# Performance work log

Measured on AMD Instinct MI355X. Metric: run time of the kernel, lower is better.

Reference implementation:

```python
import math
import jax, jax.numpy as jnp
import numpy as np

SHAPES = ((100, 150), (50, 75), (25, 38), (13, 19))  # (H, W) per level
N_HEADS = 8
N_POINTS = 4
EMBED = 256


def setup_inputs() -> dict:
    key = jax.random.key(0)
    ks = jax.random.split(key, 8)
    bs = 2
    L = len(SHAPES)
    nv = sum(h * w for h, w in SHAPES)  # 19947
    nq = nv
    d = EMBED
    query = jax.random.normal(ks[0], (bs, nq, d), jnp.float32)
    value = jax.random.normal(ks[1], (bs, nv, d), jnp.float32)
    reference_points = jax.random.uniform(ks[2], (bs, nq, L, 2), dtype=jnp.float32)
    spatial_shapes = jnp.asarray(np.array(SHAPES, np.int32))
    # sampling_offsets bias: directional grid init, as in the module's init_weights
    thetas = np.arange(N_HEADS, dtype=np.float64) * (2.0 * math.pi / N_HEADS)
    grid = np.stack([np.cos(thetas), np.sin(thetas)], -1)
    grid = grid / np.abs(grid).max(-1, keepdims=True)
    grid = np.tile(grid[:, None, None, :], (1, L, N_POINTS, 1))
    grid = grid * np.arange(1, N_POINTS + 1, dtype=np.float64)[None, None, :, None]
    b_off = jnp.asarray(grid.reshape(-1), jnp.float32)  # (h*L*p*2,)
    # small random weights (zero-init in module would make offsets constant)
    W_off = 0.01 * jax.random.normal(ks[3], (N_HEADS * L * N_POINTS * 2, d), jnp.float32)
    W_attn = 0.01 * jax.random.normal(ks[4], (N_HEADS * L * N_POINTS, d), jnp.float32)
    b_attn = jnp.zeros((N_HEADS * L * N_POINTS,), jnp.float32)
    s = 1.0 / math.sqrt(d)
    W_val = s * jax.random.normal(ks[5], (d, d), jnp.float32)
    b_val = jnp.zeros((d,), jnp.float32)
    W_out = s * jax.random.normal(ks[6], (d, d), jnp.float32)
    b_out = jnp.zeros((d,), jnp.float32)
    return dict(query=query, value=value, reference_points=reference_points,
                spatial_shapes=spatial_shapes, W_off=W_off, b_off=b_off,
                W_attn=W_attn, b_attn=b_attn, W_val=W_val, b_val=b_val,
                W_out=W_out, b_out=b_out)


def _msda(value, shapes, loc, attn):
    """Multi-scale deformable attention core.
    value: (bs, nv, h, hd)  loc: (bs, nq, h, L, p, 2) in [0,1]
    attn:  (bs, nq, h, L, p) -> returns (bs, nq, h*hd)
    Equivalent to grid_sample(bilinear, padding='zeros', align_corners=False).
    """
    bs, nq, h, L, p, _ = loc.shape
    hd = value.shape[-1]
    out = jnp.zeros((bs, nq, h, hd), value.dtype)
    start = 0
    for lvl in range(L):
        H, W = int(shapes[lvl, 0]), int(shapes[lvl, 1])
        v = value[:, start:start + H * W]               # (bs, H*W, h, hd)
        l = loc[:, :, :, lvl]                           # (bs, nq, h, p, 2)
        # align_corners=False unnormalization: x = loc*W - 0.5
        x = l[..., 0] * W - 0.5
        y = l[..., 1] * H - 0.5
        x0 = jnp.floor(x)
        y0 = jnp.floor(y)
        wx = x - x0
        wy = y - y0
        x0i = x0.astype(jnp.int32)
        y0i = y0.astype(jnp.int32)

        def corner(xi, yi, w):
            valid = (xi >= 0) & (xi < W) & (yi >= 0) & (yi < H)
            idx = jnp.clip(yi, 0, H - 1) * W + jnp.clip(xi, 0, W - 1)  # (bs,nq,h,p)
            idxf = idx.transpose(0, 1, 3, 2).reshape(bs, nq * p, h)
            g = jnp.take_along_axis(v, idxf[..., None], axis=1)        # (bs,nq*p,h,hd)
            g = g.reshape(bs, nq, p, h, hd).transpose(0, 1, 3, 2, 4)   # (bs,nq,h,p,hd)
            return g * jnp.where(valid, w, 0.0)[..., None]

        samp = (corner(x0i, y0i, (1 - wx) * (1 - wy))
                + corner(x0i + 1, y0i, wx * (1 - wy))
                + corner(x0i, y0i + 1, (1 - wx) * wy)
                + corner(x0i + 1, y0i + 1, wx * wy))
        out = out + (samp * attn[:, :, :, lvl, :, None]).sum(3)
        start += H * W
    return out.reshape(bs, nq, h * hd)


def reference(query, value, reference_points, spatial_shapes,
              W_off, b_off, W_attn, b_attn, W_val, b_val, W_out, b_out):
    shapes = np.asarray(spatial_shapes)  # static level shapes
    bs, nq, d = query.shape
    L = shapes.shape[0]
    h, p = N_HEADS, N_POINTS
    hd = d // h
    off = (query @ W_off.T + b_off).reshape(bs, nq, h, L, p, 2)
    aw = (query @ W_attn.T + b_attn).reshape(bs, nq, h, L * p)
    aw = jax.nn.softmax(aw, axis=-1).reshape(bs, nq, h, L, p)
    v = (value @ W_val.T + b_val).reshape(bs, -1, h, hd)
    # offset normalizer is (W, H) per level
    norm = jnp.asarray(np.stack([shapes[:, 1], shapes[:, 0]], -1), query.dtype)  # (L,2)
    loc = reference_points[:, :, None, :, None, :] + off / norm[None, None, None, :, None, :]
    out = _msda(v, shapes, loc, aw)          # (bs, nq, d)
    return out @ W_out.T + b_out
```

## Files before the change

kernel.cpp:

```cpp
#include <hip/hip_runtime.h>
#include <hip/hip_bf16.h>
#include <hip/hip_fp16.h>
#include <cmath>


typedef __attribute__((ext_vector_type(8))) short short8;
typedef __attribute__((ext_vector_type(4))) float f32x4;

#define MREAL 39894
#define MP    39936
#define NQ2   39894

__device__ __forceinline__ unsigned short f2bf(float f) {
    union { float f; unsigned u; } x; x.f = f;
    unsigned r = (x.u + 0x7fffu + ((x.u >> 16) & 1u)) >> 16;
    return (unsigned short)r;
}
__device__ __forceinline__ unsigned cvt_pk_bf16(float lo, float hi) {
    unsigned r;
    asm("v_cvt_pk_bf16_f32 %0, %1, %2" : "=v"(r) : "v"(lo), "v"(hi));
    return r;
}

__global__ __launch_bounds__(256) void cast_w4(
    const float* __restrict__ woff, const float* __restrict__ wattn,
    const float* __restrict__ wval, const float* __restrict__ wout,
    short* __restrict__ wb)
{
    int c = blockIdx.x * 256 + threadIdx.x;
    const float* s; short* d; int off;
    if (c < 8192)       { s = woff;  d = wb;          off = c; }
    else if (c < 12288) { s = wattn; d = wb + 65536;  off = c - 8192; }
    else if (c < 20480) { s = wval;  d = wb + 98304;  off = c - 12288; }
    else                { s = wout;  d = wb + 163840; off = c - 20480; }
    const float4* f4 = reinterpret_cast<const float4*>(s) + (size_t)off * 2;
    float4 a = f4[0], b = f4[1];
    short8 o;
    o[0] = (short)f2bf(a.x); o[1] = (short)f2bf(a.y);
    o[2] = (short)f2bf(a.z); o[3] = (short)f2bf(a.w);
    o[4] = (short)f2bf(b.x); o[5] = (short)f2bf(b.y);
    o[6] = (short)f2bf(b.z); o[7] = (short)f2bf(b.w);
    *reinterpret_cast<short8*>(d + (size_t)off * 8) = o;
}

template<int AMODE, int OUTMODE, int NT>
__global__ __launch_bounds__(256) void gemm_bf16_nt(
    const void* __restrict__ A, const short* __restrict__ B,
    const float* __restrict__ bias, const float* __restrict__ bias2, int bsplit,
    void* __restrict__ Cout, int ldc, int c0, int Mstore)
{
    __shared__ short As[128 * 40];
    __shared__ short Bs[128 * 40];

    const int bid = blockIdx.x;
    const int m_t = ((bid / (8 * NT)) << 3) | (bid & 7);
    const int n_t = (bid >> 3) % NT;
    const int m0 = m_t * 128;
    const int n0 = n_t * 128;

    const int tid = threadIdx.x;
    const int w  = tid >> 6;
    const int l  = tid & 63;
    const int wm = w >> 1, wn = w & 1;

    const int sr  = tid >> 2;
    const int skc = (tid & 3) * 8;

    const int lr = l & 15;
    const int lk = (l >> 4) * 8;

    f32x4 acc[4][4] = {};

    for (int k0 = 0; k0 < 256; k0 += 32) {
        __syncthreads();
        if constexpr (AMODE == 0) {
            const short* Ab = (const short*)A;
            *reinterpret_cast<short8*>(&As[sr * 40 + skc]) =
                *reinterpret_cast<const short8*>(&Ab[(size_t)(m0 + sr) * 256 + k0 + skc]);
            *reinterpret_cast<short8*>(&As[(sr + 64) * 40 + skc]) =
                *reinterpret_cast<const short8*>(&Ab[(size_t)(m0 + sr + 64) * 256 + k0 + skc]);
        } else {
            const float* Af = (const float*)A;
            const int r0 = min(m0 + sr, MREAL - 1);
            const int r1 = min(m0 + sr + 64, MREAL - 1);
            float4 a0 = *reinterpret_cast<const float4*>(&Af[(size_t)r0 * 256 + k0 + skc]);
            float4 a1 = *reinterpret_cast<const float4*>(&Af[(size_t)r0 * 256 + k0 + skc + 4]);
            float4 b0 = *reinterpret_cast<const float4*>(&Af[(size_t)r1 * 256 + k0 + skc]);
            float4 b1 = *reinterpret_cast<const float4*>(&Af[(size_t)r1 * 256 + k0 + skc + 4]);
            uint4 pa, pb;
            pa.x = cvt_pk_bf16(a0.x, a0.y); pa.y = cvt_pk_bf16(a0.z, a0.w);
            pa.z = cvt_pk_bf16(a1.x, a1.y); pa.w = cvt_pk_bf16(a1.z, a1.w);
            pb.x = cvt_pk_bf16(b0.x, b0.y); pb.y = cvt_pk_bf16(b0.z, b0.w);
            pb.z = cvt_pk_bf16(b1.x, b1.y); pb.w = cvt_pk_bf16(b1.z, b1.w);
            *reinterpret_cast<uint4*>(&As[sr * 40 + skc]) = pa;
            *reinterpret_cast<uint4*>(&As[(sr + 64) * 40 + skc]) = pb;
        }
        *reinterpret_cast<short8*>(&Bs[sr * 40 + skc]) =
            *reinterpret_cast<const short8*>(&B[(size_t)(n0 + sr) * 256 + k0 + skc]);
        *reinterpret_cast<short8*>(&Bs[(sr + 64) * 40 + skc]) =
            *reinterpret_cast<const short8*>(&B[(size_t)(n0 + sr + 64) * 256 + k0 + skc]);
        __syncthreads();

        short8 bfr[4];
#pragma unroll
        for (int ni = 0; ni < 4; ++ni)
            bfr[ni] = *reinterpret_cast<const short8*>(&Bs[(wn * 64 + ni * 16 + lr) * 40 + lk]);
#pragma unroll
        for (int mi = 0; mi < 4; ++mi) {
            short8 afr = *reinterpret_cast<const short8*>(&As[(wm * 64 + mi * 16 + lr) * 40 + lk]);
#pragma unroll
            for (int ni = 0; ni < 4; ++ni)
                acc[mi][ni] = __builtin_amdgcn_mfma_f32_16x16x32_bf16(afr, bfr[ni], acc[mi][ni], 0, 0, 0);
        }
    }

    const int r4 = (l >> 4) * 4;
#pragma unroll
    for (int ni = 0; ni < 4; ++ni) {
        const int col = n0 + wn * 64 + ni * 16 + lr;
        const float bv = (col < bsplit) ? bias[col] : bias2[col - bsplit];
#pragma unroll
        for (int mi = 0; mi < 4; ++mi) {
#pragma unroll
            for (int r = 0; r < 4; ++r) {
                const int row = m0 + wm * 64 + mi * 16 + r4 + r;
                if (row < Mstore) {
                    const float val = acc[mi][ni][r] + bv;
                    if constexpr (OUTMODE == 2) {
                        union { __half h; unsigned short u; } cv; cv.h = __float2half(val);
                        reinterpret_cast<unsigned short*>(Cout)[(size_t)row * ldc + c0 + col] = cv.u;
                    } else if constexpr (OUTMODE == 3) {
                        union { __half h; unsigned short u; } cv; cv.h = __float2half(val);
                        reinterpret_cast<unsigned short*>(Cout)[(size_t)(col >> 5) * MP * 32
                                                               + (size_t)row * 32 + (col & 31)] = cv.u;
                    } else {
                        reinterpret_cast<float*>(Cout)[(size_t)row * ldc + c0 + col] = val;
                    }
                }
            }
        }
    }
}

__global__ __launch_bounds__(256) void msda_sample6(
    const char* __restrict__ vplanes,
    const __half* __restrict__ offattn,
    const float* __restrict__ ref,
    uint4* __restrict__ sampled)
{
    __shared__ __attribute__((aligned(16))) unsigned s_w[16][68];
    __shared__ __attribute__((aligned(16))) int      s_idx[16][68];
    __shared__ float s_e[16][17];
    __shared__ float s_inv[16];

    const int bid = blockIdx.x;
    const int h = bid & 7;
    const int qbase = (bid >> 3) * 16;
    const int tid = threadIdx.x;
    const int qp = tid >> 4;

    {
        const int s = tid & 15;
        const int lvl = s >> 2;
        const int qi = qbase + qp;
        const bool live = (qi < NQ2);

        const int Hs[4] = {100, 50, 25, 13};
        const int Ws[4] = {150, 75, 38, 19};
        const int st[4] = {0, 15000, 18750, 19700};

        float e = 1.f;
        unsigned wv[4] = {0, 0, 0, 0};
        int      iv[4] = {0, 0, 0, 0};
        if (live) {
            const __half* oa = offattn + (size_t)qi * 384;
            unsigned short lu = __builtin_nontemporal_load(
                reinterpret_cast<const unsigned short*>(oa + 256 + h * 16 + s));
            union { unsigned short u; __half h; } lh; lh.u = lu;
            e = expf(__half2float(lh.h));
            unsigned ou = __builtin_nontemporal_load(
                reinterpret_cast<const unsigned*>(oa + h * 32 + 2 * s));
            union { unsigned u; __half2 h2; } oh; oh.u = ou;
            const float ox = __low2float(oh.h2), oy = __high2float(oh.h2);
            const float2 r2 = *reinterpret_cast<const float2*>(ref + (size_t)qi * 8 + lvl * 2);

            const int H = Hs[lvl], W = Ws[lvl];
            const float x = r2.x * (float)W + ox - 0.5f;
            const float y = r2.y * (float)H + oy - 0.5f;
            const float x0f = floorf(x), y0f = floorf(y);
            const float wx = x - x0f, wy = y - y0f;
            const int x0 = (int)x0f, y0 = (int)y0f;
            const int base = ((qi >= 19947) ? 19947 : 0) + st[lvl];

            const float w00 = (1.f - wx) * (1.f - wy), w01 = wx * (1.f - wy);
            const float w10 = (1.f - wx) * wy,         w11 = wx * wy;
            const bool vx0 = (x0 >= 0) & (x0 < W), vx1 = (x0 + 1 >= 0) & (x0 + 1 < W);
            const bool vy0 = (y0 >= 0) & (y0 < H), vy1 = (y0 + 1 >= 0) & (y0 + 1 < H);
            const int xc0 = min(max(x0, 0), W - 1), xc1 = min(max(x0 + 1, 0), W - 1);
            const int yc0 = min(max(y0, 0), H - 1), yc1 = min(max(y0 + 1, 0), H - 1);
            iv[0] = (base + yc0 * W + xc0) << 6;
            iv[1] = (base + yc0 * W + xc1) << 6;
            iv[2] = (base + yc1 * W + xc0) << 6;
            iv[3] = (base + yc1 * W + xc1) << 6;
            union { __half2 h; unsigned u; } cw;
            cw.h = __float2half2_rn((vx0 & vy0) ? e * w00 : 0.f); wv[0] = cw.u;
            cw.h = __float2half2_rn((vx1 & vy0) ? e * w01 : 0.f); wv[1] = cw.u;
            cw.h = __float2half2_rn((vx0 & vy1) ? e * w10 : 0.f); wv[2] = cw.u;
            cw.h = __float2half2_rn((vx1 & vy1) ? e * w11 : 0.f); wv[3] = cw.u;
        }
        s_e[qp][s] = e;
#pragma unroll
        for (int c = 0; c < 4; ++c) {
            s_w[qp][c * 16 + s] = wv[c];
            s_idx[qp][c * 16 + s] = iv[c];
        }
    }
    __syncthreads();

    if (tid < 16) {
        float d = 0.f;
#pragma unroll
        for (int i = 0; i < 16; ++i) d += s_e[tid][i];
        s_inv[tid] = 1.f / d;
    }
    __syncthreads();

    const int l = tid & 63;
    const int c4 = (l >> 2) & 3;
    const int cp4 = l & 3;
    const int qi = qbase + qp;

    const char* vb = vplanes + (size_t)h * (MP * 64) + cp4 * 16;

    union HU { __half2 h; unsigned u; };
    __half2 acc[4];
#pragma unroll
    for (int i = 0; i < 4; ++i) acc[i] = __float2half2_rn(0.f);

    const unsigned* wp = &s_w[qp][c4 * 16];
    const int*      ip = &s_idx[qp][c4 * 16];

#pragma unroll
    for (int k = 0; k < 4; ++k) {
        const uint4 w4 = *reinterpret_cast<const uint4*>(wp + k * 4);
        const int4  i4 = *reinterpret_cast<const int4*>(ip + k * 4);
        const uint4 p0 = *reinterpret_cast<const uint4*>(vb + i4.x);
        const uint4 p1 = *reinterpret_cast<const uint4*>(vb + i4.y);
        const uint4 p2 = *reinterpret_cast<const uint4*>(vb + i4.z);
        const uint4 p3 = *reinterpret_cast<const uint4*>(vb + i4.w);
        HU va, ww;
        ww.u = w4.x;
        va.u = p0.x; acc[0] = __hfma2(va.h, ww.h, acc[0]);
        va.u = p0.y; acc[1] = __hfma2(va.h, ww.h, acc[1]);
        va.u = p0.z; acc[2] = __hfma2(va.h, ww.h, acc[2]);
        va.u = p0.w; acc[3] = __hfma2(va.h, ww.h, acc[3]);
        ww.u = w4.y;
        va.u = p1.x; acc[0] = __hfma2(va.h, ww.h, acc[0]);
        va.u = p1.y; acc[1] = __hfma2(va.h, ww.h, acc[1]);
        va.u = p1.z; acc[2] = __hfma2(va.h, ww.h, acc[2]);
        va.u = p1.w; acc[3] = __hfma2(va.h, ww.h, acc[3]);
        ww.u = w4.z;
        va.u = p2.x; acc[0] = __hfma2(va.h, ww.h, acc[0]);
        va.u = p2.y; acc[1] = __hfma2(va.h, ww.h, acc[1]);
        va.u = p2.z; acc[2] = __hfma2(va.h, ww.h, acc[2]);
        va.u = p2.w; acc[3] = __hfma2(va.h, ww.h, acc[3]);
        ww.u = w4.w;
        va.u = p3.x; acc[0] = __hfma2(va.h, ww.h, acc[0]);
        va.u = p3.y; acc[1] = __hfma2(va.h, ww.h, acc[1]);
        va.u = p3.z; acc[2] = __hfma2(va.h, ww.h, acc[2]);
        va.u = p3.w; acc[3] = __hfma2(va.h, ww.h, acc[3]);
    }

#pragma unroll
    for (int i = 0; i < 4; ++i) {
        HU a; a.h = acc[i];
        HU b;
        b.u = __shfl_xor(a.u, 4, 64); a.h = __hadd2(a.h, b.h);
        b.u = __shfl_xor(a.u, 8, 64); a.h = __hadd2(a.h, b.h);
        acc[i] = a.h;
    }

    if (c4 == 0 && qi < NQ2) {
        const float inv = s_inv[qp];
        uint4 o;
        o.x = ((unsigned)f2bf(__high2float(acc[0]) * inv) << 16) | (unsigned)f2bf(__low2float(acc[0]) * inv);
        o.y = ((unsigned)f2bf(__high2float(acc[1]) * inv) << 16) | (unsigned)f2bf(__low2float(acc[1]) * inv);
        o.z = ((unsigned)f2bf(__high2float(acc[2]) * inv) << 16) | (unsigned)f2bf(__low2float(acc[2]) * inv);
        o.w = ((unsigned)f2bf(__high2float(acc[3]) * inv) << 16) | (unsigned)f2bf(__low2float(acc[3]) * inv);
        sampled[(size_t)qi * 32 + h * 4 + cp4] = o;
    }
}

extern "C" void kernel_launch(void* const* d_in, const int* in_sizes, int n_in,
                              void* d_out, int out_size, void* d_ws, size_t ws_size,
                              hipStream_t stream) {
    const float* query  = (const float*)d_in[0];
    const float* value  = (const float*)d_in[1];
    const float* refp   = (const float*)d_in[2];
    const float* W_off  = (const float*)d_in[4];
    const float* b_off  = (const float*)d_in[5];
    const float* W_attn = (const float*)d_in[6];
    const float* b_attn = (const float*)d_in[7];
    const float* W_val  = (const float*)d_in[8];
    const float* b_val  = (const float*)d_in[9];
    const float* W_out  = (const float*)d_in[10];
    const float* b_out  = (const float*)d_in[11];
    float* out = (float*)d_out;

    short* wb    = (short*)d_ws;
    short* vbuf  = wb + 262144;
    short* oabuf = vbuf + (size_t)MP * 256;
    short* sbuf  = oabuf + (size_t)MP * 384;

    const dim3 blk(256);

    cast_w4<<<dim3(112), blk, 0, stream>>>(W_off, W_attn, W_val, W_out, wb);

    gemm_bf16_nt<1, 3, 2><<<dim3(312 * 2), blk, 0, stream>>>(
        value, wb + 98304, b_val, b_val, 1 << 30, vbuf, 256, 0, MP);
    gemm_bf16_nt<1, 2, 3><<<dim3(312 * 3), blk, 0, stream>>>(
        query, wb, b_off, b_attn, 256, oabuf, 384, 0, MP);

    const int ngroups = (MREAL + 15) / 16;
    msda_sample6<<<dim3(ngroups * 8), blk, 0, stream>>>(
        (const char*)vbuf, (const __half*)oabuf, refp, (uint4*)sbuf);

    gemm_bf16_nt<0, 0, 2><<<dim3(312 * 2), blk, 0, stream>>>(
        sbuf, wb + 163840, b_out, b_out, 1 << 30, out, 256, 0, MREAL);
}
```

Baseline: 170.7 us.

## Fuse weight casting into GEMMs, merge input GEMMs, streamline sampling kernel

Drops the separate weight-cast kernel: the GEMMs now load fp32 weights and convert them to bf16 while staging into shared memory. The value and query projections run as one launch that dispatches on block index. In the sampling kernel, the softmax denominator is now a wave shuffle reduction instead of a shared-memory pass with an extra barrier, expf becomes __expf, and all 16 gathers are issued before any FMAs to raise memory-level parallelism. The cost is redundant fp32 weight loads and conversions in every GEMM block, plus more live registers in the sampler.

```diff
diff --git a/kernel.cpp b/kernel.cpp
--- a/kernel.cpp
+++ b/kernel.cpp
@@ -22,43 +22,16 @@
     return r;
 }
 
-__global__ __launch_bounds__(256) void cast_w4(
-    const float* __restrict__ woff, const float* __restrict__ wattn,
-    const float* __restrict__ wval, const float* __restrict__ wout,
-    short* __restrict__ wb)
+template<int AMODE, int OUTMODE>
+__device__ __forceinline__ void gemm_body(
+    short* As, short* Bs,
+    const void* A, const float* B1, const float* B2, int nsplit,
+    const float* bias, const float* bias2, int bsplit,
+    void* Cout, int ldc, int m_t, int n_t, int Mstore)
 {
-    int c = blockIdx.x * 256 + threadIdx.x;
-    const float* s; short* d; int off;
-    if (c < 8192)       { s = woff;  d = wb;          off = c; }
-    else if (c < 12288) { s = wattn; d = wb + 65536;  off = c - 8192; }
-    else if (c < 20480) { s = wval;  d = wb + 98304;  off = c - 12288; }
-    else                { s = wout;  d = wb + 163840; off = c - 20480; }
-    const float4* f4 = reinterpret_cast<const float4*>(s) + (size_t)off * 2;
-    float4 a = f4[0], b = f4[1];
-    short8 o;
-    o[0] = (short)f2bf(a.x); o[1] = (short)f2bf(a.y);
-    o[2] = (short)f2bf(a.z); o[3] = (short)f2bf(a.w);
-    o[4] = (short)f2bf(b.x); o[5] = (short)f2bf(b.y);
-    o[6] = (short)f2bf(b.z); o[7] = (short)f2bf(b.w);
-    *reinterpret_cast<short8*>(d + (size_t)off * 8) = o;
-}
-
-template<int AMODE, int OUTMODE, int NT>
-__global__ __launch_bounds__(256) void gemm_bf16_nt(
-    const void* __restrict__ A, const short* __restrict__ B,
-    const float* __restrict__ bias, const float* __restrict__ bias2, int bsplit,
-    void* __restrict__ Cout, int ldc, int c0, int Mstore)
-{
-    __shared__ short As[128 * 40];
-    __shared__ short Bs[128 * 40];
-
-    const int bid = blockIdx.x;
-    const int m_t = ((bid / (8 * NT)) << 3) | (bid & 7);
-    const int n_t = (bid >> 3) % NT;
+    const int tid = threadIdx.x;
     const int m0 = m_t * 128;
     const int n0 = n_t * 128;
-
-    const int tid = threadIdx.x;
     const int w  = tid >> 6;
     const int l  = tid & 63;
     const int wm = w >> 1, wn = w & 1;
@@ -68,6 +41,12 @@
 
     const int lr = l & 15;
     const int lk = (l >> 4) * 8;
+
+    const int br0 = n0 + sr, br1 = n0 + sr + 64;
+    const float* Bp0 = (br0 < nsplit) ? B1 + (size_t)br0 * 256
+                                      : B2 + (size_t)(br0 - nsplit) * 256;
+    const float* Bp1 = (br1 < nsplit) ? B1 + (size_t)br1 * 256
+                                      : B2 + (size_t)(br1 - nsplit) * 256;
 
     f32x4 acc[4][4] = {};
 
@@ -95,10 +74,19 @@
             *reinterpret_cast<uint4*>(&As[sr * 40 + skc]) = pa;
             *reinterpret_cast<uint4*>(&As[(sr + 64) * 40 + skc]) = pb;
         }
-        *reinterpret_cast<short8*>(&Bs[sr * 40 + skc]) =
-            *reinterpret_cast<const short8*>(&B[(size_t)(n0 + sr) * 256 + k0 + skc]);
-        *reinterpret_cast<short8*>(&Bs[(sr + 64) * 40 + skc]) =
-            *reinterpret_cast<const short8*>(&B[(size_t)(n0 + sr + 64) * 256 + k0 + skc]);
+        {
+            float4 c0 = *reinterpret_cast<const float4*>(Bp0 + k0 + skc);
+            float4 c1 = *reinterpret_cast<const float4*>(Bp0 + k0 + skc + 4);
+            float4 d0 = *reinterpret_cast<const float4*>(Bp1 + k0 + skc);
+            float4 d1 = *reinterpret_cast<const float4*>(Bp1 + k0 + skc + 4);
+            uint4 pc, pd;
+            pc.x = cvt_pk_bf16(c0.x, c0.y); pc.y = cvt_pk_bf16(c0.z, c0.w);
+            pc.z = cvt_pk_bf16(c1.x, c1.y); pc.w = cvt_pk_bf16(c1.z, c1.w);
+            pd.x = cvt_pk_bf16(d0.x, d0.y); pd.y = cvt_pk_bf16(d0.z, d0.w);
+            pd.z = cvt_pk_bf16(d1.x, d1.y); pd.w = cvt_pk_bf16(d1.z, d1.w);
+            *reinterpret_cast<uint4*>(&Bs[sr * 40 + skc]) = pc;
+            *reinterpret_cast<uint4*>(&Bs[(sr + 64) * 40 + skc]) = pd;
+        }
         __syncthreads();
 
         short8 bfr[4];
@@ -128,13 +116,13 @@
                     const float val = acc[mi][ni][r] + bv;
                     if constexpr (OUTMODE == 2) {
                         union { __half h; unsigned short u; } cv; cv.h = __float2half(val);
-                        reinterpret_cast<unsigned short*>(Cout)[(size_t)row * ldc + c0 + col] = cv.u;
+                        reinterpret_cast<unsigned short*>(Cout)[(size_t)row * ldc + col] = cv.u;
                     } else if constexpr (OUTMODE == 3) {
                         union { __half h; unsigned short u; } cv; cv.h = __float2half(val);
                         reinterpret_cast<unsigned short*>(Cout)[(size_t)(col >> 5) * MP * 32
                                                                + (size_t)row * 32 + (col & 31)] = cv.u;
                     } else {
-                        reinterpret_cast<float*>(Cout)[(size_t)row * ldc + c0 + col] = val;
+                        reinterpret_cast<float*>(Cout)[(size_t)row * ldc + col] = val;
                     }
                 }
             }
@@ -142,7 +130,46 @@
     }
 }
 
-__global__ __launch_bounds__(256) void msda_sample6(
+__global__ __launch_bounds__(256) void gemm_fused(
+    const float* __restrict__ value, const float* __restrict__ query,
+    const float* __restrict__ woff, const float* __restrict__ wattn,
+    const float* __restrict__ wval,
+    const float* __restrict__ b_off, const float* __restrict__ b_attn,
+    const float* __restrict__ b_val,
+    short* __restrict__ vplanes, short* __restrict__ oabuf)
+{
+    __shared__ short As[128 * 40];
+    __shared__ short Bs[128 * 40];
+
+    const int bid = blockIdx.x;
+    if (bid < 624) {
+        const int m_t = ((bid >> 4) << 3) | (bid & 7);
+        const int n_t = (bid >> 3) & 1;
+        gemm_body<1, 3>(As, Bs, value, wval, wval, 256,
+                        b_val, b_val, 1 << 30, vplanes, 256, m_t, n_t, MP);
+    } else {
+        const int b = bid - 624;
+        const int m_t = ((b / 24) << 3) | (b & 7);
+        const int n_t = (b >> 3) % 3;
+        gemm_body<1, 2>(As, Bs, query, woff, wattn, 256,
+                        b_off, b_attn, 256, oabuf, 384, m_t, n_t, MP);
+    }
+}
+
+__global__ __launch_bounds__(256) void gemm_out(
+    const short* __restrict__ sbuf, const float* __restrict__ wout,
+    const float* __restrict__ b_out, float* __restrict__ out)
+{
+    __shared__ short As[128 * 40];
+    __shared__ short Bs[128 * 40];
+    const int bid = blockIdx.x;
+    const int m_t = ((bid >> 4) << 3) | (bid & 7);
+    const int n_t = (bid >> 3) & 1;
+    gemm_body<0, 0>(As, Bs, sbuf, wout, wout, 256,
+                    b_out, b_out, 1 << 30, out, 256, m_t, n_t, MREAL);
+}
+
+__global__ __launch_bounds__(256) void msda_sample7(
     const char* __restrict__ vplanes,
     const __half* __restrict__ offattn,
     const float* __restrict__ ref,
@@ -150,7 +177,6 @@
 {
     __shared__ __attribute__((aligned(16))) unsigned s_w[16][68];
     __shared__ __attribute__((aligned(16))) int      s_idx[16][68];
-    __shared__ float s_e[16][17];
     __shared__ float s_inv[16];
 
     const int bid = blockIdx.x;
@@ -177,7 +203,7 @@
             unsigned short lu = __builtin_nontemporal_load(
                 reinterpret_cast<const unsigned short*>(oa + 256 + h * 16 + s));
             union { unsigned short u; __half h; } lh; lh.u = lu;
-            e = expf(__half2float(lh.h));
+            e = __expf(__half2float(lh.h));
             unsigned ou = __builtin_nontemporal_load(
                 reinterpret_cast<const unsigned*>(oa + h * 32 + 2 * s));
             union { unsigned u; __half2 h2; } oh; oh.u = ou;
@@ -208,20 +234,17 @@
             cw.h = __float2half2_rn((vx0 & vy1) ? e * w10 : 0.f); wv[2] = cw.u;
             cw.h = __float2half2_rn((vx1 & vy1) ? e * w11 : 0.f); wv[3] = cw.u;
         }
-        s_e[qp][s] = e;
+        float den = e;
+        den += __shfl_xor(den, 1, 64);
+        den += __shfl_xor(den, 2, 64);
+        den += __shfl_xor(den, 4, 64);
+        den += __shfl_xor(den, 8, 64);
+        if (s == 0) s_inv[qp] = 1.f / den;
 #pragma unroll
         for (int c = 0; c < 4; ++c) {
             s_w[qp][c * 16 + s] = wv[c];
             s_idx[qp][c * 16 + s] = iv[c];
         }
-    }
-    __syncthreads();
-
-    if (tid < 16) {
-        float d = 0.f;
-#pragma unroll
-        for (int i = 0; i < 16; ++i) d += s_e[tid][i];
-        s_inv[tid] = 1.f / d;
     }
     __syncthreads();
 
@@ -232,44 +255,51 @@
 
     const char* vb = vplanes + (size_t)h * (MP * 64) + cp4 * 16;
 
+    const unsigned* wp = &s_w[qp][c4 * 16];
+    const int*      ip = &s_idx[qp][c4 * 16];
+
+    const int4 ia = *reinterpret_cast<const int4*>(ip + 0);
+    const int4 ib = *reinterpret_cast<const int4*>(ip + 4);
+    const int4 ic = *reinterpret_cast<const int4*>(ip + 8);
+    const int4 id = *reinterpret_cast<const int4*>(ip + 12);
+    const uint4 wa = *reinterpret_cast<const uint4*>(wp + 0);
+    const uint4 wb = *reinterpret_cast<const uint4*>(wp + 4);
+    const uint4 wc = *reinterpret_cast<const uint4*>(wp + 8);
+    const uint4 wd = *reinterpret_cast<const uint4*>(wp + 12);
+
+    const uint4 p0  = *reinterpret_cast<const uint4*>(vb + ia.x);
+    const uint4 p1  = *reinterpret_cast<const uint4*>(vb + ia.y);
+    const uint4 p2  = *reinterpret_cast<const uint4*>(vb + ia.z);
+    const uint4 p3  = *reinterpret_cast<const uint4*>(vb + ia.w);
+    const uint4 p4  = *reinterpret_cast<const uint4*>(vb + ib.x);
+    const uint4 p5  = *reinterpret_cast<const uint4*>(vb + ib.y);
+    const uint4 p6  = *reinterpret_cast<const uint4*>(vb + ib.z);
+    const uint4 p7  = *reinterpret_cast<const uint4*>(vb + ib.w);
+    const uint4 p8  = *reinterpret_cast<const uint4*>(vb + ic.x);
+    const uint4 p9  = *reinterpret_cast<const uint4*>(vb + ic.y);
+    const uint4 p10 = *reinterpret_cast<const uint4*>(vb + ic.z);
+    const uint4 p11 = *reinterpret_cast<const uint4*>(vb + ic.w);
+    const uint4 p12 = *reinterpret_cast<const uint4*>(vb + id.x);
+    const uint4 p13 = *reinterpret_cast<const uint4*>(vb + id.y);
+    const uint4 p14 = *reinterpret_cast<const uint4*>(vb + id.z);
+    const uint4 p15 = *reinterpret_cast<const uint4*>(vb + id.w);
+
     union HU { __half2 h; unsigned u; };
     __half2 acc[4];
 #pragma unroll
     for (int i = 0; i < 4; ++i) acc[i] = __float2half2_rn(0.f);
 
-    const unsigned* wp = &s_w[qp][c4 * 16];
-    const int*      ip = &s_idx[qp][c4 * 16];
-
-#pragma unroll
-    for (int k = 0; k < 4; ++k) {
-        const uint4 w4 = *reinterpret_cast<const uint4*>(wp + k * 4);
-        const int4  i4 = *reinterpret_cast<const int4*>(ip + k * 4);
-        const uint4 p0 = *reinterpret_cast<const uint4*>(vb + i4.x);
-        const uint4 p1 = *reinterpret_cast<const uint4*>(vb + i4.y);
-        const uint4 p2 = *reinterpret_cast<const uint4*>(vb + i4.z);
-        const uint4 p3 = *reinterpret_cast<const uint4*>(vb + i4.w);
-        HU va, ww;
-        ww.u = w4.x;
-        va.u = p0.x; acc[0] = __hfma2(va.h, ww.h, acc[0]);
-        va.u = p0.y; acc[1] = __hfma2(va.h, ww.h, acc[1]);
-        va.u = p0.z; acc[2] = __hfma2(va.h, ww.h, acc[2]);
-        va.u = p0.w; acc[3] = __hfma2(va.h, ww.h, acc[3]);
-        ww.u = w4.y;
-        va.u = p1.x; acc[0] = __hfma2(va.h, ww.h, acc[0]);
-        va.u = p1.y; acc[1] = __hfma2(va.h, ww.h, acc[1]);
-        va.u = p1.z; acc[2] = __hfma2(va.h, ww.h, acc[2]);
-        va.u = p1.w; acc[3] = __hfma2(va.h, ww.h, acc[3]);
-        ww.u = w4.z;
-        va.u = p2.x; acc[0] = __hfma2(va.h, ww.h, acc[0]);
-        va.u = p2.y; acc[1] = __hfma2(va.h, ww.h, acc[1]);
-        va.u = p2.z; acc[2] = __hfma2(va.h, ww.h, acc[2]);
-        va.u = p2.w; acc[3] = __hfma2(va.h, ww.h, acc[3]);
-        ww.u = w4.w;
-        va.u = p3.x; acc[0] = __hfma2(va.h, ww.h, acc[0]);
-        va.u = p3.y; acc[1] = __hfma2(va.h, ww.h, acc[1]);
-        va.u = p3.z; acc[2] = __hfma2(va.h, ww.h, acc[2]);
-        va.u = p3.w; acc[3] = __hfma2(va.h, ww.h, acc[3]);
-    }
+#define FMA4(P, WU) { HU va, ww; ww.u = (WU); \
+    va.u = (P).x; acc[0] = __hfma2(va.h, ww.h, acc[0]); \
+    va.u = (P).y; acc[1] = __hfma2(va.h, ww.h, acc[1]); \
+    va.u = (P).z; acc[2] = __hfma2(va.h, ww.h, acc[2]); \
+    va.u = (P).w; acc[3] = __hfma2(va.h, ww.h, acc[3]); }
+
+    FMA4(p0,  wa.x) FMA4(p1,  wa.y) FMA4(p2,  wa.z) FMA4(p3,  wa.w)
+    FMA4(p4,  wb.x) FMA4(p5,  wb.y) FMA4(p6,  wb.z) FMA4(p7,  wb.w)
+    FMA4(p8,  wc.x) FMA4(p9,  wc.y) FMA4(p10, wc.z) FMA4(p11, wc.w)
+    FMA4(p12, wd.x) FMA4(p13, wd.y) FMA4(p14, wd.z) FMA4(p15, wd.w)
+#undef FMA4
 
 #pragma unroll
     for (int i = 0; i < 4; ++i) {
@@ -307,24 +337,18 @@
     const float* b_out  = (const float*)d_in[11];
     float* out = (float*)d_out;
 
-    short* wb    = (short*)d_ws;
-    short* vbuf  = wb + 262144;
-    short* oabuf = vbuf + (size_t)MP * 256;
-    short* sbuf  = oabuf + (size_t)MP * 384;
+    short* vplanes = (short*)d_ws;
+    short* oabuf   = vplanes + (size_t)MP * 256;
+    short* sbuf    = oabuf + (size_t)MP * 384;
 
     const dim3 blk(256);
 
-    cast_w4<<<dim3(112), blk, 0, stream>>>(W_off, W_attn, W_val, W_out, wb);
-
-    gemm_bf16_nt<1, 3, 2><<<dim3(312 * 2), blk, 0, stream>>>(
-        value, wb + 98304, b_val, b_val, 1 << 30, vbuf, 256, 0, MP);
-    gemm_bf16_nt<1, 2, 3><<<dim3(312 * 3), blk, 0, stream>>>(
-        query, wb, b_off, b_attn, 256, oabuf, 384, 0, MP);
+    gemm_fused<<<dim3(624 + 936), blk, 0, stream>>>(
+        value, query, W_off, W_attn, W_val, b_off, b_attn, b_val, vplanes, oabuf);
 
     const int ngroups = (MREAL + 15) / 16;
-    msda_sample6<<<dim3(ngroups * 8), blk, 0, stream>>>(
-        (const char*)vbuf, (const __half*)oabuf, refp, (uint4*)sbuf);
-
-    gemm_bf16_nt<0, 0, 2><<<dim3(312 * 2), blk, 0, stream>>>(
-        sbuf, wb + 163840, b_out, b_out, 1 << 30, out, 256, 0, MREAL);
-}
+    msda_sample7<<<dim3(ngroups * 8), blk, 0, stream>>>(
+        (const char*)vplanes, (const __half*)oabuf, refp, (uint4*)sbuf);
+
+    gemm_out<<<dim3(624), blk, 0, stream>>>(sbuf, W_out, b_out, out);
+}
```

Measured after the change: 140.0 us. -18.0%, faster.
